# Kernel tuning notes

Measured on AMD Instinct MI355X. Metric: run time of the kernel, lower is better.

## Reference

```python
import jax, jax.numpy as jnp
import numpy as np

B, K, C = 16384, 128, 32  # batch, feature dim, number of private-label classes
LN2 = 0.6931471805599453


def setup_inputs() -> dict:
    key = jax.random.key(0)
    k1, k2, k3 = jax.random.split(key, 3)
    feature = jax.random.normal(k1, (B, K), dtype=jnp.float32)
    privatelabel = jax.random.randint(k2, (B,), 0, C)
    pan = jax.random.normal(k3, (1,), dtype=jnp.float32)  # unused by the module
    return {"feature": feature, "privatelabel": privatelabel, "pan": pan}


def _privacy_loss(feature, privatelabel):
    b, k = feature.shape
    labels = privatelabel
    onehot = jax.nn.one_hot(labels, C, dtype=feature.dtype)          # [B,C]
    counts = onehot.sum(axis=0)                                      # [C]
    mu = (onehot.T @ feature) / counts[:, None]                      # [C,K] per-class mean
    xc = feature - mu[labels]                                        # [B,K] centered rows
    # per-class scatter: S_c = (1/n_c) * sum_{i in c} xc_i xc_i^T + I
    xw = xc[:, None, :] * onehot[:, :, None]                         # [B,C,K]
    S = jnp.einsum('bci,bj->cij', xw, xc) / counts[:, None, None]
    S = S + jnp.eye(k, dtype=feature.dtype)                          # Sigma_a = I
    # pairwise Gaussian KL (with log base 2, as in the torch code)
    ld2 = jnp.linalg.slogdet(S)[1] / LN2                             # log2 det Sigma_c
    inv = jnp.linalg.inv(S)                                          # [C,K,K]
    diff = mu[:, None, :] - mu[None, :, :]                           # [C,C,K] (i,j)
    quad = jnp.einsum('ijk,jkl,ijl->ij', diff, inv, diff)           # (u1-u2)^T S2^-1 (u1-u2)
    tr = jnp.einsum('jab,iba->ij', inv, S)                           # trace(S2^-1 S1)
    kl = 0.5 * ((ld2[None, :] - ld2[:, None]) - float(k) + quad + tr)
    # dict-insertion key order = order of first occurrence of each label;
    # loops are i in [0, C-2] (rows), j in [1, C-1] (cols) over that order
    first = jnp.full((C,), b, dtype=jnp.int32).at[labels].min(
        jnp.arange(b, dtype=jnp.int32))
    rank = jnp.argsort(jnp.argsort(first))                           # appearance rank per class
    mask = (rank[:, None] <= C - 2) & (rank[None, :] >= 1)
    result = -jnp.sum(mu * mu) + jnp.sum(jnp.where(mask, kl, jnp.zeros_like(kl)))
    return result[None]                                              # shape (1,), like torch


def reference(feature, privatelabel, pan):
    return _privacy_loss(feature, privatelabel)
```

## Files before the change

kernel.cpp:

```cpp
#include <hip/hip_runtime.h>

#define B_ROWS 16384
#define K_DIM  128
#define C_CLS  32

#define O_COUNTS   0
#define O_FIRST    256
#define O_RANK     512
#define O_LD2      1152
#define O_COLSUM   2048
#define O_MU       18432
#define O_S        102400
#define O_PART     (102400 + 2097152)
#define O_INV      O_PART

__global__ __launch_bounds__(256) void k_init(int* __restrict__ counts,
    int* __restrict__ first, float* __restrict__ colsum, float* __restrict__ out) {
  const int t = threadIdx.x;
  if (t < C_CLS) { counts[t] = 0; first[t] = 0x7fffffff; }
  if (t == 0) out[0] = 0.f;
  for (int i = t; i < C_CLS * K_DIM; i += 256) colsum[i] = 0.f;
}

template<int NSPLIT>
__global__ __launch_bounds__(256) void k_scatter(const float* __restrict__ feat,
    const int* __restrict__ label, int* __restrict__ counts, int* __restrict__ first,
    float* __restrict__ part, float* __restrict__ colsum) {
  constexpr int CH = B_ROWS / NSPLIT;
  const int c = blockIdx.x / NSPLIT, s = blockIdx.x % NSPLIT;
  __shared__ int lls[CH];
  __shared__ int lcnt;
  __shared__ __align__(16) float ls[32 * 128];
  const int t = threadIdx.x;
  if (t == 0) lcnt = 0;
  __syncthreads();
  int myMin = 0x7fffffff;
  const int lane = t & 63;
  for (int r0 = 0; r0 < CH; r0 += 256) {
    const int i = s * CH + r0 + t;
    const bool match = (label[i] == c);
    unsigned long long mask = __ballot(match);
    int prefix = __popcll(mask & ((1ull << lane) - 1ull));
    int wcnt = __popcll(mask);
    int base = 0;
    if (lane == 0 && wcnt) base = atomicAdd(&lcnt, wcnt);
    base = __shfl(base, 0);
    if (match) { lls[base + prefix] = i; myMin = min(myMin, i); }
  }
  #pragma unroll
  for (int off = 32; off > 0; off >>= 1) myMin = min(myMin, __shfl_xor(myMin, off));
  if (lane == 0 && myMin != 0x7fffffff) atomicMin(&first[c], myMin);
  __syncthreads();
  const int n = lcnt;
  if (t == 0) atomicAdd(&counts[c], n);

  const int tr = t >> 4, tc = t & 15;
  float acc[8][8];
  #pragma unroll
  for (int i = 0; i < 8; ++i)
    #pragma unroll
    for (int j = 0; j < 8; ++j) acc[i][j] = 0.f;
  float cs = 0.f;
  const int col = t & 127, half = t >> 7;
  for (int base2 = 0; base2 < n; base2 += 32) {
    const int nb = min(32, n - base2);
    __syncthreads();
    #pragma unroll
    for (int w = 0; w < 4; ++w) {
      int f4 = w * 256 + t;
      int r = f4 >> 5, c4 = f4 & 31;
      float4 v = make_float4(0.f, 0.f, 0.f, 0.f);
      if (r < nb) {
        int row = lls[base2 + r];
        v = ((const float4*)(feat + (long)row * K_DIM))[c4];
      }
      ((float4*)ls)[f4] = v;
    }
    __syncthreads();
    #pragma unroll
    for (int r0 = 0; r0 < 16; ++r0) cs += ls[(half * 16 + r0) * 128 + col];
    for (int r = 0; r < nb; ++r) {
      const float4* lr = (const float4*)(ls + r * 128);
      float4 A0 = lr[tr * 2], A1 = lr[tr * 2 + 1];
      float4 B0 = lr[tc * 2], B1 = lr[tc * 2 + 1];
      float av[8] = {A0.x, A0.y, A0.z, A0.w, A1.x, A1.y, A1.z, A1.w};
      float bv[8] = {B0.x, B0.y, B0.z, B0.w, B1.x, B1.y, B1.z, B1.w};
      #pragma unroll
      for (int i = 0; i < 8; ++i)
        #pragma unroll
        for (int j = 0; j < 8; ++j) acc[i][j] += av[i] * bv[j];
    }
  }
  float* Pc = part + (long)blockIdx.x * 16384;
  #pragma unroll
  for (int i = 0; i < 8; ++i) {
    float4* prow = (float4*)(Pc + (tr * 8 + i) * 128);
    prow[tc * 2]     = make_float4(acc[i][0], acc[i][1], acc[i][2], acc[i][3]);
    prow[tc * 2 + 1] = make_float4(acc[i][4], acc[i][5], acc[i][6], acc[i][7]);
  }
  atomicAdd(&colsum[c * 128 + col], cs);
}

template<int NSPLIT>
__global__ __launch_bounds__(1024) void k_sweepf(const float* __restrict__ part,
    const float* __restrict__ colsum, const int* __restrict__ counts,
    const int* __restrict__ first, float* __restrict__ S, float* __restrict__ INVg,
    float* __restrict__ mu, int* __restrict__ rank_g, float* __restrict__ ld2) {
  const int c = blockIdx.x, t = threadIdx.x;
  __shared__ __align__(16) float ml[128];
  __shared__ __align__(16) float vbuf[2][132];
  const float n = (float)counts[c];
  const float rn = 1.0f / n;
  if (t < 128) {
    float m = colsum[c * 128 + t] * rn;
    ml[t] = m;
    mu[c * 128 + t] = m;
  }
  if (t == 0) {
    const int f = first[c];
    int r = 0;
    for (int c2 = 0; c2 < C_CLS; ++c2) {
      const int f2 = first[c2];
      r += (f2 < f) || (f2 == f && c2 < c);
    }
    rank_g[c] = r;
  }
  __syncthreads();
  const int h = t >> 5, c4i = t & 31;
  float4 A[4];
  float4* S4 = (float4*)(S + c * 16384);
  #pragma unroll
  for (int q = 0; q < 4; ++q) {
    const int f4 = q * 1024 + t;
    float4 v = make_float4(0.f, 0.f, 0.f, 0.f);
    #pragma unroll
    for (int k = 0; k < NSPLIT; ++k) {
      const float4 p = ((const float4*)(part + (long)(c * NSPLIT + k) * 16384))[f4];
      v.x += p.x; v.y += p.y; v.z += p.z; v.w += p.w;
    }
    const int row = q * 32 + h;
    const float mr = ml[row];
    const float4 mc = ((const float4*)ml)[c4i];
    const int b = 4 * c4i;
    v.x = v.x * rn - mr * mc.x + ((row == b + 0) ? 1.f : 0.f);
    v.y = v.y * rn - mr * mc.y + ((row == b + 1) ? 1.f : 0.f);
    v.z = v.z * rn - mr * mc.z + ((row == b + 2) ? 1.f : 0.f);
    v.w = v.w * rn - mr * mc.w + ((row == b + 3) ? 1.f : 0.f);
    A[q] = v;
    S4[f4] = v;
  }
  float lda = 0.f;
  for (int P = 0; P < 128; ++P) {
    float* vb = vbuf[P & 1];
    if (h == (P & 31)) {
      const int qexp = P >> 5;
      float4 ex = A[0];
      #pragma unroll
      for (int q = 1; q < 4; ++q) if (q == qexp) ex = A[q];
      if (c4i == (P >> 2)) {
        const int e = P & 3;
        float dv = (e == 0) ? ex.x : (e == 1) ? ex.y : (e == 2) ? ex.z : ex.w;
        vb[128] = dv;
        if (e == 0) ex.x -= 1.f; else if (e == 1) ex.y -= 1.f;
        else if (e == 2) ex.z -= 1.f; else ex.w -= 1.f;
      }
      ((float4*)vb)[c4i] = ex;
    }
    __syncthreads();
    const float d = vb[128];
    const float dinv = 1.0f / d;
    lda += __log2f(d);
    const float4 vc = ((const float4*)vb)[c4i];
    const float4 wc = make_float4(vc.x * dinv, vc.y * dinv, vc.z * dinv, vc.w * dinv);
    #pragma unroll
    for (int q = 0; q < 4; ++q) {
      const float vr = vb[q * 32 + h];
      A[q].x -= vr * wc.x;
      A[q].y -= vr * wc.y;
      A[q].z -= vr * wc.z;
      A[q].w -= vr * wc.w;
    }
  }
  float4* O4 = (float4*)(INVg + c * 16384);
  const int e = h & 3;
  #pragma unroll
  for (int q = 0; q < 4; ++q) {
    const int rq = q * 32 + h;
    const float pf = (c4i == (rq >> 2)) ? 2.f : 0.f;
    float4 o;
    o.x = ((e == 0) ? pf : 0.f) - A[q].x;
    o.y = ((e == 1) ? pf : 0.f) - A[q].y;
    o.z = ((e == 2) ? pf : 0.f) - A[q].z;
    o.w = ((e == 3) ? pf : 0.f) - A[q].w;
    O4[q * 1024 + t] = o;
  }
  if (t == 0) ld2[c] = lda;
}

__global__ __launch_bounds__(256) void k_pairs(const float* __restrict__ S,
    const float* __restrict__ INVg, const float* __restrict__ mu,
    const float* __restrict__ ld2, const int* __restrict__ rank_g,
    float* __restrict__ out) {
  const int j = blockIdx.x, i = blockIdx.y;
  const int t = threadIdx.x;
  __shared__ __align__(16) float dl[128];
  __shared__ float wsum[4];
  if (i == 0 && j == 0) {
    float s2 = 0.f;
    #pragma unroll
    for (int q = 0; q < 16; ++q) { float m = mu[q * 256 + t]; s2 += m * m; }
    #pragma unroll
    for (int off = 32; off > 0; off >>= 1) s2 += __shfl_xor(s2, off);
    if ((t & 63) == 0) wsum[t >> 6] = s2;
    __syncthreads();
    if (t == 0) atomicAdd(out, -(wsum[0] + wsum[1] + wsum[2] + wsum[3]));
    __syncthreads();
  }
  if (rank_g[i] > C_CLS - 2 || rank_g[j] < 1) return;
  if (t < 128) dl[t] = mu[i * 128 + t] - mu[j * 128 + t];
  __syncthreads();
  const float4* Si4 = (const float4*)(S + i * 16384);
  const float4* Ij4 = (const float4*)(INVg + j * 16384);
  float s = 0.f;
  #pragma unroll
  for (int q = 0; q < 16; ++q) {
    int f4 = q * 256 + t;
    int a = f4 >> 5, b4 = f4 & 31;
    float da = dl[a];
    float4 db = ((const float4*)dl)[b4];
    float4 si = Si4[f4], ij = Ij4[f4];
    s += ij.x * (si.x + da * db.x);
    s += ij.y * (si.y + da * db.y);
    s += ij.z * (si.z + da * db.z);
    s += ij.w * (si.w + da * db.w);
  }
  #pragma unroll
  for (int off = 32; off > 0; off >>= 1) s += __shfl_xor(s, off);
  if ((t & 63) == 0) wsum[t >> 6] = s;
  __syncthreads();
  if (t == 0) {
    float tot = wsum[0] + wsum[1] + wsum[2] + wsum[3];
    float kl = 0.5f * ((ld2[j] - ld2[i]) - 128.0f + tot);
    atomicAdd(out, kl);
  }
}

extern "C" void kernel_launch(void* const* d_in, const int* in_sizes, int n_in,
                              void* d_out, int out_size, void* d_ws, size_t ws_size,
                              hipStream_t stream) {
  const float* feat  = (const float*)d_in[0];
  const int*   label = (const int*)d_in[1];
  float* out = (float*)d_out;
  char*  ws  = (char*)d_ws;

  int*   counts  = (int*)(ws + O_COUNTS);
  int*   first   = (int*)(ws + O_FIRST);
  int*   rank_g  = (int*)(ws + O_RANK);
  float* ld2     = (float*)(ws + O_LD2);
  float* colsum  = (float*)(ws + O_COLSUM);
  float* mu      = (float*)(ws + O_MU);
  float* S       = (float*)(ws + O_S);
  float* part    = (float*)(ws + O_PART);
  float* INVg    = (float*)(ws + O_INV);

  const size_t need8 = (size_t)O_PART + (size_t)C_CLS * 8 * 65536;

  k_init<<<1, 256, 0, stream>>>(counts, first, colsum, out);
  if (ws_size >= need8) {
    k_scatter<8><<<C_CLS * 8, 256,  0, stream>>>(feat, label, counts, first, part, colsum);
    k_sweepf<8> <<<C_CLS,     1024, 0, stream>>>(part, colsum, counts, first, S, INVg, mu, rank_g, ld2);
  } else {
    k_scatter<4><<<C_CLS * 4, 256,  0, stream>>>(feat, label, counts, first, part, colsum);
    k_sweepf<4> <<<C_CLS,     1024, 0, stream>>>(part, colsum, counts, first, S, INVg, mu, rank_g, ld2);
  }
  k_pairs<<<dim3(C_CLS, C_CLS), 256, 0, stream>>>(S, INVg, mu, ld2, rank_g, out);
}
```

Measured before the change: 159.6 us.

## Drop init kernel via per-block partials and pipeline Gauss-Jordan pivot row

Removes the separate init kernel and the global atomics for counts, first-occurrence and column sums. Each scatter block now writes its own partial values, which the sweep kernel reduces; the output is zeroed in the sweep kernel. The Gauss-Jordan loop is restructured so the next pivot row is computed during the current update, which leaves one barrier per pivot step instead of a serialized extract-then-sync. The inverse is written into the first slot of each class's partial buffer, and k_pairs now takes a stride argument to read it.

```diff
diff --git a/kernel.cpp b/kernel.cpp
--- a/kernel.cpp
+++ b/kernel.cpp
@@ -4,35 +4,29 @@
 #define K_DIM  128
 #define C_CLS  32
 
-#define O_COUNTS   0
-#define O_FIRST    256
-#define O_RANK     512
-#define O_LD2      1152
-#define O_COLSUM   2048
-#define O_MU       18432
-#define O_S        102400
-#define O_PART     (102400 + 2097152)
-#define O_INV      O_PART
-
-__global__ __launch_bounds__(256) void k_init(int* __restrict__ counts,
-    int* __restrict__ first, float* __restrict__ colsum, float* __restrict__ out) {
-  const int t = threadIdx.x;
-  if (t < C_CLS) { counts[t] = 0; first[t] = 0x7fffffff; }
-  if (t == 0) out[0] = 0.f;
-  for (int i = t; i < C_CLS * K_DIM; i += 256) colsum[i] = 0.f;
-}
+#define O_COUNTSP 0
+#define O_FIRSTP  1024
+#define O_RANK    2048
+#define O_LD2     2304
+#define O_MU      2560
+#define O_COLSUMP 20480
+#define O_S       151552
+#define O_PART    2248704
 
 template<int NSPLIT>
 __global__ __launch_bounds__(256) void k_scatter(const float* __restrict__ feat,
-    const int* __restrict__ label, int* __restrict__ counts, int* __restrict__ first,
-    float* __restrict__ part, float* __restrict__ colsum) {
+    const int* __restrict__ label, int* __restrict__ counts_p,
+    int* __restrict__ first_p, float* __restrict__ part,
+    float* __restrict__ colsum_p) {
   constexpr int CH = B_ROWS / NSPLIT;
-  const int c = blockIdx.x / NSPLIT, s = blockIdx.x % NSPLIT;
+  const int bid = blockIdx.x;
+  const int c = bid / NSPLIT, s = bid % NSPLIT;
   __shared__ int lls[CH];
-  __shared__ int lcnt;
+  __shared__ int lcnt, lmin;
   __shared__ __align__(16) float ls[32 * 128];
+  __shared__ float lcs[256];
   const int t = threadIdx.x;
-  if (t == 0) lcnt = 0;
+  if (t == 0) { lcnt = 0; lmin = 0x7fffffff; }
   __syncthreads();
   int myMin = 0x7fffffff;
   const int lane = t & 63;
@@ -49,10 +43,10 @@
   }
   #pragma unroll
   for (int off = 32; off > 0; off >>= 1) myMin = min(myMin, __shfl_xor(myMin, off));
-  if (lane == 0 && myMin != 0x7fffffff) atomicMin(&first[c], myMin);
+  if (lane == 0) atomicMin(&lmin, myMin);
   __syncthreads();
   const int n = lcnt;
-  if (t == 0) atomicAdd(&counts[c], n);
+  if (t == 0) { counts_p[bid] = n; first_p[bid] = lmin; }
 
   const int tr = t >> 4, tc = t & 15;
   float acc[8][8];
@@ -91,41 +85,55 @@
         for (int j = 0; j < 8; ++j) acc[i][j] += av[i] * bv[j];
     }
   }
-  float* Pc = part + (long)blockIdx.x * 16384;
+  float* Pc = part + (long)bid * 16384;
   #pragma unroll
   for (int i = 0; i < 8; ++i) {
     float4* prow = (float4*)(Pc + (tr * 8 + i) * 128);
     prow[tc * 2]     = make_float4(acc[i][0], acc[i][1], acc[i][2], acc[i][3]);
     prow[tc * 2 + 1] = make_float4(acc[i][4], acc[i][5], acc[i][6], acc[i][7]);
   }
-  atomicAdd(&colsum[c * 128 + col], cs);
+  lcs[t] = cs;
+  __syncthreads();
+  if (t < 128) colsum_p[bid * 128 + t] = lcs[t] + lcs[t + 128];
 }
 
 template<int NSPLIT>
-__global__ __launch_bounds__(1024) void k_sweepf(const float* __restrict__ part,
-    const float* __restrict__ colsum, const int* __restrict__ counts,
-    const int* __restrict__ first, float* __restrict__ S, float* __restrict__ INVg,
-    float* __restrict__ mu, int* __restrict__ rank_g, float* __restrict__ ld2) {
+__global__ __launch_bounds__(1024) void k_sweepf(float* __restrict__ part,
+    const float* __restrict__ colsum_p, const int* __restrict__ counts_p,
+    const int* __restrict__ first_p, float* __restrict__ S,
+    float* __restrict__ mu, int* __restrict__ rank_g, float* __restrict__ ld2,
+    float* __restrict__ out) {
   const int c = blockIdx.x, t = threadIdx.x;
   __shared__ __align__(16) float ml[128];
   __shared__ __align__(16) float vbuf[2][132];
-  const float n = (float)counts[c];
-  const float rn = 1.0f / n;
+  __shared__ int lfirst[C_CLS];
+  if (c == 0 && t == 0) out[0] = 0.f;
+  int n = 0;
+  #pragma unroll
+  for (int k = 0; k < NSPLIT; ++k) n += counts_p[c * NSPLIT + k];
+  const float rn = 1.0f / (float)n;
   if (t < 128) {
-    float m = colsum[c * 128 + t] * rn;
+    float m = 0.f;
+    #pragma unroll
+    for (int k = 0; k < NSPLIT; ++k) m += colsum_p[(c * NSPLIT + k) * 128 + t];
+    m *= rn;
     ml[t] = m;
     mu[c * 128 + t] = m;
   }
+  if (t < C_CLS) {
+    int f = 0x7fffffff;
+    #pragma unroll
+    for (int k = 0; k < NSPLIT; ++k) f = min(f, first_p[t * NSPLIT + k]);
+    lfirst[t] = f;
+  }
+  __syncthreads();
   if (t == 0) {
-    const int f = first[c];
+    const int f = lfirst[c];
     int r = 0;
-    for (int c2 = 0; c2 < C_CLS; ++c2) {
-      const int f2 = first[c2];
-      r += (f2 < f) || (f2 == f && c2 < c);
-    }
+    for (int c2 = 0; c2 < C_CLS; ++c2)
+      r += (lfirst[c2] < f) || (lfirst[c2] == f && c2 < c);
     rank_g[c] = r;
   }
-  __syncthreads();
   const int h = t >> 5, c4i = t & 31;
   float4 A[4];
   float4* S4 = (float4*)(S + c * 16384);
@@ -149,29 +157,41 @@
     A[q] = v;
     S4[f4] = v;
   }
+  if (h == 0) {
+    float4 ex = A[0];
+    if (c4i == 0) { vbuf[0][128] = ex.x; ex.x -= 1.f; }
+    ((float4*)vbuf[0])[c4i] = ex;
+  }
+  __syncthreads();
   float lda = 0.f;
   for (int P = 0; P < 128; ++P) {
-    float* vb = vbuf[P & 1];
-    if (h == (P & 31)) {
-      const int qexp = P >> 5;
-      float4 ex = A[0];
-      #pragma unroll
-      for (int q = 1; q < 4; ++q) if (q == qexp) ex = A[q];
-      if (c4i == (P >> 2)) {
-        const int e = P & 3;
-        float dv = (e == 0) ? ex.x : (e == 1) ? ex.y : (e == 2) ? ex.z : ex.w;
-        vb[128] = dv;
-        if (e == 0) ex.x -= 1.f; else if (e == 1) ex.y -= 1.f;
-        else if (e == 2) ex.z -= 1.f; else ex.w -= 1.f;
-      }
-      ((float4*)vb)[c4i] = ex;
-    }
-    __syncthreads();
+    const float* vb = vbuf[P & 1];
+    float* vbn = vbuf[(P + 1) & 1];
     const float d = vb[128];
     const float dinv = 1.0f / d;
     lda += __log2f(d);
     const float4 vc = ((const float4*)vb)[c4i];
     const float4 wc = make_float4(vc.x * dinv, vc.y * dinv, vc.z * dinv, vc.w * dinv);
+    if (P < 127 && h == ((P + 1) & 31)) {
+      const int qn = (P + 1) >> 5;
+      const float vrn = vb[P + 1];
+      float4 aq = A[0];
+      #pragma unroll
+      for (int q = 1; q < 4; ++q) if (q == qn) aq = A[q];
+      float4 ex;
+      ex.x = aq.x - vrn * wc.x;
+      ex.y = aq.y - vrn * wc.y;
+      ex.z = aq.z - vrn * wc.z;
+      ex.w = aq.w - vrn * wc.w;
+      if (c4i == ((P + 1) >> 2)) {
+        const int e = (P + 1) & 3;
+        const float dv = (e == 0) ? ex.x : (e == 1) ? ex.y : (e == 2) ? ex.z : ex.w;
+        vbn[128] = dv;
+        if (e == 0) ex.x -= 1.f; else if (e == 1) ex.y -= 1.f;
+        else if (e == 2) ex.z -= 1.f; else ex.w -= 1.f;
+      }
+      ((float4*)vbn)[c4i] = ex;
+    }
     #pragma unroll
     for (int q = 0; q < 4; ++q) {
       const float vr = vb[q * 32 + h];
@@ -180,8 +200,9 @@
       A[q].z -= vr * wc.z;
       A[q].w -= vr * wc.w;
     }
-  }
-  float4* O4 = (float4*)(INVg + c * 16384);
+    __syncthreads();
+  }
+  float4* O4 = (float4*)(part + (long)c * NSPLIT * 16384);
   const int e = h & 3;
   #pragma unroll
   for (int q = 0; q < 4; ++q) {
@@ -198,9 +219,9 @@
 }
 
 __global__ __launch_bounds__(256) void k_pairs(const float* __restrict__ S,
-    const float* __restrict__ INVg, const float* __restrict__ mu,
-    const float* __restrict__ ld2, const int* __restrict__ rank_g,
-    float* __restrict__ out) {
+    const float* __restrict__ INVg, const long invStride,
+    const float* __restrict__ mu, const float* __restrict__ ld2,
+    const int* __restrict__ rank_g, float* __restrict__ out) {
   const int j = blockIdx.x, i = blockIdx.y;
   const int t = threadIdx.x;
   __shared__ __align__(16) float dl[128];
@@ -220,7 +241,7 @@
   if (t < 128) dl[t] = mu[i * 128 + t] - mu[j * 128 + t];
   __syncthreads();
   const float4* Si4 = (const float4*)(S + i * 16384);
-  const float4* Ij4 = (const float4*)(INVg + j * 16384);
+  const float4* Ij4 = (const float4*)(INVg + (long)j * invStride);
   float s = 0.f;
   #pragma unroll
   for (int q = 0; q < 16; ++q) {
@@ -253,25 +274,24 @@
   float* out = (float*)d_out;
   char*  ws  = (char*)d_ws;
 
-  int*   counts  = (int*)(ws + O_COUNTS);
-  int*   first   = (int*)(ws + O_FIRST);
-  int*   rank_g  = (int*)(ws + O_RANK);
-  float* ld2     = (float*)(ws + O_LD2);
-  float* colsum  = (float*)(ws + O_COLSUM);
-  float* mu      = (float*)(ws + O_MU);
-  float* S       = (float*)(ws + O_S);
-  float* part    = (float*)(ws + O_PART);
-  float* INVg    = (float*)(ws + O_INV);
+  int*   counts_p = (int*)(ws + O_COUNTSP);
+  int*   first_p  = (int*)(ws + O_FIRSTP);
+  int*   rank_g   = (int*)(ws + O_RANK);
+  float* ld2      = (float*)(ws + O_LD2);
+  float* mu       = (float*)(ws + O_MU);
+  float* colsum_p = (float*)(ws + O_COLSUMP);
+  float* S        = (float*)(ws + O_S);
+  float* part     = (float*)(ws + O_PART);
 
   const size_t need8 = (size_t)O_PART + (size_t)C_CLS * 8 * 65536;
 
-  k_init<<<1, 256, 0, stream>>>(counts, first, colsum, out);
   if (ws_size >= need8) {
-    k_scatter<8><<<C_CLS * 8, 256,  0, stream>>>(feat, label, counts, first, part, colsum);
-    k_sweepf<8> <<<C_CLS,     1024, 0, stream>>>(part, colsum, counts, first, S, INVg, mu, rank_g, ld2);
+    k_scatter<8><<<C_CLS * 8, 256,  0, stream>>>(feat, label, counts_p, first_p, part, colsum_p);
+    k_sweepf<8> <<<C_CLS,     1024, 0, stream>>>(part, colsum_p, counts_p, first_p, S, mu, rank_g, ld2, out);
+    k_pairs     <<<dim3(C_CLS, C_CLS), 256, 0, stream>>>(S, part, (long)8 * 16384, mu, ld2, rank_g, out);
   } else {
-    k_scatter<4><<<C_CLS * 4, 256,  0, stream>>>(feat, label, counts, first, part, colsum);
-    k_sweepf<4> <<<C_CLS,     1024, 0, stream>>>(part, colsum, counts, first, S, INVg, mu, rank_g, ld2);
-  }
-  k_pairs<<<dim3(C_CLS, C_CLS), 256, 0, stream>>>(S, INVg, mu, ld2, rank_g, out);
-}
+    k_scatter<4><<<C_CLS * 4, 256,  0, stream>>>(feat, label, counts_p, first_p, part, colsum_p);
+    k_sweepf<4> <<<C_CLS,     1024, 0, stream>>>(part, colsum_p, counts_p, first_p, S, mu, rank_g, ld2, out);
+    k_pairs     <<<dim3(C_CLS, C_CLS), 256, 0, stream>>>(S, part, (long)4 * 16384, mu, ld2, rank_g, out);
+  }
+}
```

Measured after the change: 152.5 us. 1.05x faster.
